# Performance work log

Measured on AMD Instinct MI355X. Metric: run time of the kernel, lower is better.

## Reference

```python
import jax, jax.numpy as jnp
import numpy as np

D_STATE = 16
D_CONV = 4


def rmsnorm(x, w, eps=1e-6):
    # normalize over last (channel) axis
    return x * jax.lax.rsqrt(jnp.mean(x * x, axis=-1, keepdims=True) + eps) * w


def silu(x):
    return x * jax.nn.sigmoid(x)


def mamba(x, in_proj_w, conv1d_w, conv1d_b, x_proj_w, dt_proj_w, dt_proj_b, A_log, D_param, out_proj_w):
    # x: [B, L, C], d_inner == C (expand=1)
    B, L, C = x.shape
    dt_rank = dt_proj_w.shape[1]
    xz = jnp.einsum('blc,ec->ble', x, in_proj_w)  # [B, L, 2C]
    u, z = jnp.split(xz, 2, axis=-1)
    # causal depthwise conv1d over time (pad left d_conv-1)
    uc = jax.lax.conv_general_dilated(
        u.transpose(0, 2, 1), conv1d_w[:, None, :], (1,), [(D_CONV - 1, 0)],
        dimension_numbers=('NCH', 'OIH', 'NCH'), feature_group_count=C)
    u = silu((uc + conv1d_b[None, :, None]).transpose(0, 2, 1))  # [B, L, C]
    x_dbl = jnp.einsum('blc,ec->ble', u, x_proj_w)  # [B, L, dt_rank + 2*N]
    dt, Bm, Cm = jnp.split(x_dbl, [dt_rank, dt_rank + D_STATE], axis=-1)
    delta = jax.nn.softplus(jnp.einsum('blr,dr->bld', dt, dt_proj_w) + dt_proj_b)  # [B, L, C]
    A = -jnp.exp(A_log)  # [C, N]
    deltaA = jnp.exp(delta[..., None] * A)              # [B, L, C, N]
    deltaBu = (delta * u)[..., None] * Bm[:, :, None, :]  # [B, L, C, N]

    def step(h, inp):
        dA, dBu, c = inp
        h = dA * h + dBu
        return h, jnp.einsum('bdn,bn->bd', h, c)

    h0 = jnp.zeros((B, C, D_STATE), x.dtype)
    _, ys = jax.lax.scan(step, h0, (deltaA.transpose(1, 0, 2, 3),
                                    deltaBu.transpose(1, 0, 2, 3),
                                    Cm.transpose(1, 0, 2)))
    y = ys.transpose(1, 0, 2) + u * D_param  # [B, L, C]
    y = y * silu(z)
    return jnp.einsum('bld,od->blo', y, out_proj_w)


def reference(x, norm_w, in_proj_w, conv1d_w, conv1d_b, x_proj_w, dt_proj_w, dt_proj_b,
              A_log, D_param, out_proj_w, scale_mod, dw_w, dw_b, res_scale):
    B, C, H, W = x.shape
    x_cl = x.transpose(0, 2, 3, 1)              # [B, H, W, C]
    xn_cl = rmsnorm(x_cl, norm_w)
    x_norm = xn_cl.transpose(0, 3, 1, 2)        # [B, C, H, W]
    # bidirectional Mamba over flattened spatial sequence
    x_flat = xn_cl.reshape(B, H * W, C)
    mparams = (in_proj_w, conv1d_w, conv1d_b, x_proj_w, dt_proj_w, dt_proj_b, A_log, D_param, out_proj_w)
    fwd = mamba(x_flat, *mparams)
    bwd = jnp.flip(mamba(jnp.flip(x_flat, axis=1), *mparams), axis=1)
    g = (fwd + bwd) * scale_mod
    global_feat = g.reshape(B, H, W, C).transpose(0, 3, 1, 2)
    # local spatial gating: sigmoid(depthwise 3x3 conv) * x_norm
    conv = jax.lax.conv_general_dilated(
        x_norm, dw_w[:, None, :, :], (1, 1), [(1, 1), (1, 1)],
        dimension_numbers=('NCHW', 'OIHW', 'NCHW'), feature_group_count=C)
    local_feat = jax.nn.sigmoid(conv + dw_b[None, :, None, None]) * x_norm
    return x + res_scale * (global_feat + local_feat)


def setup_inputs() -> dict:
    key = jax.random.key(0)
    ks = jax.random.split(key, 10)
    B, C, H, W = 8, 384, 32, 32
    dt_rank = 24  # ceil(384 / 16)
    s = 0.02
    f32 = jnp.float32
    return {
        'x': jax.random.normal(ks[0], (B, C, H, W), f32),
        'norm_w': jnp.ones((C,), f32),
        'in_proj_w': jax.random.normal(ks[1], (2 * C, C), f32) * s,
        'conv1d_w': jax.random.normal(ks[2], (C, D_CONV), f32) * 0.2,
        'conv1d_b': jnp.zeros((C,), f32),
        'x_proj_w': jax.random.normal(ks[3], (dt_rank + 2 * D_STATE, C), f32) * s,
        'dt_proj_w': jax.random.normal(ks[4], (C, dt_rank), f32) * 0.1,
        'dt_proj_b': jax.random.uniform(ks[5], (C,), f32, -4.0, -2.0),
        'A_log': jnp.log(jnp.tile(jnp.arange(1, D_STATE + 1, dtype=f32), (C, 1))),
        'D_param': jnp.ones((C,), f32),
        'out_proj_w': jax.random.normal(ks[6], (C, C), f32) * s,
        'scale_mod': jnp.full((1,), 0.25, f32),
        'dw_w': jax.random.normal(ks[7], (C, 3, 3), f32) * 0.1,
        'dw_b': jnp.zeros((C,), f32),
        'res_scale': jnp.full((1,), 0.5, f32),
    }
```

## Files before the change

kernel.cpp:

```cpp
#include <hip/hip_runtime.h>
#include <hip/hip_bf16.h>


typedef __attribute__((ext_vector_type(8))) short bf16x8;
typedef __attribute__((ext_vector_type(8))) unsigned short u16x8;
typedef __attribute__((ext_vector_type(4))) float f32x4;

#define L2E 1.44269504088896340736f

static __device__ __forceinline__ unsigned short f2bf(float f) {
  unsigned int u = __builtin_bit_cast(unsigned int, f);
  u += 0x7fff + ((u >> 16) & 1);
  return (unsigned short)(u >> 16);
}
static __device__ __forceinline__ float bf2f(unsigned short u) {
  unsigned int v = (unsigned int)u << 16;
  return __builtin_bit_cast(float, v);
}

#define GLOAD_LDS16(g, l)                                             \
  __builtin_amdgcn_global_load_lds(                                   \
      (const __attribute__((address_space(1))) unsigned int*)(g),     \
      (__attribute__((address_space(3))) unsigned int*)(l), 16, 0, 0)

__global__ __launch_bounds__(256) void prep_k(
    const float* __restrict__ in_w, const float* __restrict__ x_w,
    const float* __restrict__ dt_w, const float* __restrict__ out_w,
    const float* __restrict__ A_log, const float* __restrict__ nw,
    unsigned short* __restrict__ W_in, unsigned short* __restrict__ W_x,
    unsigned short* __restrict__ W_dt, unsigned short* __restrict__ W_out,
    float* __restrict__ A2) {
  int idx = blockIdx.x * 256 + threadIdx.x;
  switch (blockIdx.y) {
    case 0: if (idx < 768 * 384) W_in[idx] = f2bf(in_w[idx] * nw[idx % 384]); break;
    case 1: if (idx < 64 * 384) { int n = idx / 384, k = idx - n * 384;
              W_x[idx] = f2bf(n < 56 ? x_w[n * 384 + k] : 0.f); } break;
    case 2: if (idx < 384 * 32) { int n = idx >> 5, k = idx & 31;
              W_dt[idx] = f2bf(k < 24 ? dt_w[n * 24 + k] : 0.f); } break;
    case 3: if (idx < 384 * 384) W_out[idx] = f2bf(out_w[idx]); break;
    case 4: if (idx < 384 * 16) A2[idx] = -expf(A_log[idx]) * L2E; break;
  }
}

__global__ __launch_bounds__(256) void transpose_k(
    const float* __restrict__ x, unsigned short* __restrict__ xb,
    float* __restrict__ nf) {
  const int b = blockIdx.y;
  const int l0 = blockIdx.x * 32;
  const int tid = threadIdx.x;
  const int cr = tid >> 5, lw = tid & 31;
  const int cj = tid & 63, lr = tid >> 6;
  __shared__ float t64[64][33];
  __shared__ float part[8][33];
  float acc = 0.f;
  for (int cc = 0; cc < 6; ++cc) {
    #pragma unroll
    for (int k = 0; k < 8; ++k) {
      int cp = k * 8 + cr;
      int c = cc * 64 + cp;
      float v = x[(((size_t)(b * 384 + c)) << 10) + l0 + lw];
      t64[cp][lw] = v;
      acc = fmaf(v, v, acc);
    }
    __syncthreads();
    #pragma unroll
    for (int k2 = 0; k2 < 8; ++k2) {
      int ll = lr + 4 * k2;
      xb[((size_t)((b << 10) + l0 + ll)) * 384 + cc * 64 + cj] = f2bf(t64[cj][ll]);
    }
    __syncthreads();
  }
  part[cr][lw] = acc;
  __syncthreads();
  if (tid < 32) {
    float s = part[0][tid] + part[1][tid] + part[2][tid] + part[3][tid] +
              part[4][tid] + part[5][tid] + part[6][tid] + part[7][tid];
    nf[(b << 10) + l0 + tid] = rsqrtf(s * (1.f / 384.f) + 1e-6f);
  }
}

template <int EPI, int SUMIN>
__global__ __launch_bounds__(256) void gemm128_k(
    const unsigned short* __restrict__ A0u, const unsigned short* __restrict__ A1u,
    const unsigned short* __restrict__ Bw, int K, int N,
    float* __restrict__ outf, unsigned short* __restrict__ outb,
    const float* __restrict__ aux) {
  __shared__ __attribute__((aligned(16))) unsigned short As[128 * 32];
  __shared__ __attribute__((aligned(16))) unsigned short Bs[128 * 32];
  const int n0 = blockIdx.x * 128, m0 = blockIdx.y * 128;
  const int tid = threadIdx.x;
  const int lane = tid & 63, wave = tid >> 6;
  const int wm = wave >> 1, wn = wave & 1;
  const int fr = lane & 15, ks = (lane >> 4) * 8;
  const int row = tid >> 2, colseg = (tid & 3) * 8;
  const unsigned short* pA0 = A0u + (size_t)(m0 + row) * K + colseg;
  const unsigned short* pA1 = A0u + (size_t)(m0 + 64 + row) * K + colseg;
  const unsigned short* pB0 = Bw + (size_t)(n0 + row) * K + colseg;
  const unsigned short* pB1 = Bw + (size_t)(n0 + 64 + row) * K + colseg;
  unsigned short* lA0 = As + wave * 512;
  unsigned short* lA1 = As + 2048 + wave * 512;
  unsigned short* lB0 = Bs + wave * 512;
  unsigned short* lB1 = Bs + 2048 + wave * 512;
  f32x4 acc[4][4] = {};
  for (int k0 = 0; k0 < K; k0 += 32) {
    __syncthreads();
    if (SUMIN) {
      #pragma unroll
      for (int p = 0; p < 2; ++p) {
        int r = p * 64 + row;
        u16x8 va = *(const u16x8*)&A0u[(size_t)(m0 + r) * K + k0 + colseg];
        u16x8 vb = *(const u16x8*)&A1u[(size_t)(m0 + r) * K + k0 + colseg];
        u16x8 s;
        #pragma unroll
        for (int j = 0; j < 8; ++j) s[j] = f2bf(bf2f(va[j]) + bf2f(vb[j]));
        *(u16x8*)&As[r * 32 + colseg] = s;
      }
    } else {
      GLOAD_LDS16(pA0, lA0);
      GLOAD_LDS16(pA1, lA1);
      pA0 += 32; pA1 += 32;
    }
    GLOAD_LDS16(pB0, lB0);
    GLOAD_LDS16(pB1, lB1);
    pB0 += 32; pB1 += 32;
    __syncthreads();
    bf16x8 af[4], bf[4];
    #pragma unroll
    for (int mi = 0; mi < 4; ++mi)
      af[mi] = *(const bf16x8*)&As[(wm * 64 + mi * 16 + fr) * 32 + ks];
    #pragma unroll
    for (int ni = 0; ni < 4; ++ni)
      bf[ni] = *(const bf16x8*)&Bs[(wn * 64 + ni * 16 + fr) * 32 + ks];
    #pragma unroll
    for (int mi = 0; mi < 4; ++mi)
      #pragma unroll
      for (int ni = 0; ni < 4; ++ni)
        acc[mi][ni] = __builtin_amdgcn_mfma_f32_16x16x32_bf16(af[mi], bf[ni], acc[mi][ni], 0, 0, 0);
  }
  #pragma unroll
  for (int mi = 0; mi < 4; ++mi)
    #pragma unroll
    for (int ni = 0; ni < 4; ++ni)
      #pragma unroll
      for (int j = 0; j < 4; ++j) {
        int m = m0 + wm * 64 + mi * 16 + (lane >> 4) * 4 + j;
        int n = n0 + wn * 64 + ni * 16 + fr;
        float v = acc[mi][ni][j];
        if (EPI == 0) {
          outb[(size_t)m * N + n] = f2bf(v * aux[m]);
        } else {
          outf[(size_t)m * N + n] = v * aux[0];
        }
      }
}

template <int EPI>
__global__ __launch_bounds__(256) void gemm_k(
    const unsigned short* __restrict__ A0u, const unsigned short* __restrict__ A1u,
    const unsigned short* __restrict__ Bw, int K, int N,
    float* __restrict__ of0, float* __restrict__ of1,
    unsigned short* __restrict__ ob0, unsigned short* __restrict__ ob1,
    const float* __restrict__ aux) {
  const unsigned short* A = blockIdx.z ? A1u : A0u;
  float* outf = blockIdx.z ? of1 : of0;
  unsigned short* outb = blockIdx.z ? ob1 : ob0;
  __shared__ unsigned short As[64][40];
  __shared__ unsigned short Bs[64][40];
  const int n0 = blockIdx.x * 64, m0 = blockIdx.y * 64;
  const int tid = threadIdx.x;
  const int lane = tid & 63, wave = tid >> 6;
  const int wm = wave >> 1, wn = wave & 1;
  const int lrow = tid >> 2, lseg = (tid & 3) * 8;
  const int fr = lane & 15, ks = (lane >> 4) * 8;
  f32x4 acc[2][2] = {};
  for (int k0 = 0; k0 < K; k0 += 32) {
    __syncthreads();
    *(bf16x8*)&As[lrow][lseg] = *(const bf16x8*)&A[(size_t)(m0 + lrow) * K + k0 + lseg];
    *(bf16x8*)&Bs[lrow][lseg] = *(const bf16x8*)&Bw[(size_t)(n0 + lrow) * K + k0 + lseg];
    __syncthreads();
    bf16x8 a0 = *(const bf16x8*)&As[wm * 32 + fr][ks];
    bf16x8 a1 = *(const bf16x8*)&As[wm * 32 + 16 + fr][ks];
    bf16x8 b0 = *(const bf16x8*)&Bs[wn * 32 + fr][ks];
    bf16x8 b1 = *(const bf16x8*)&Bs[wn * 32 + 16 + fr][ks];
    acc[0][0] = __builtin_amdgcn_mfma_f32_16x16x32_bf16(a0, b0, acc[0][0], 0, 0, 0);
    acc[0][1] = __builtin_amdgcn_mfma_f32_16x16x32_bf16(a0, b1, acc[0][1], 0, 0, 0);
    acc[1][0] = __builtin_amdgcn_mfma_f32_16x16x32_bf16(a1, b0, acc[1][0], 0, 0, 0);
    acc[1][1] = __builtin_amdgcn_mfma_f32_16x16x32_bf16(a1, b1, acc[1][1], 0, 0, 0);
  }
  #pragma unroll
  for (int mi = 0; mi < 2; ++mi)
    #pragma unroll
    for (int ni = 0; ni < 2; ++ni)
      #pragma unroll
      for (int j = 0; j < 4; ++j) {
        int m = m0 + wm * 32 + mi * 16 + (lane >> 4) * 4 + j;
        int n = n0 + wn * 32 + ni * 16 + (lane & 15);
        float v = acc[mi][ni][j];
        if (EPI == 1) {
          if (n < 24) outb[m * 32 + n] = f2bf(v);
          else if (n < 32) outb[m * 32 + n] = 0;
          if (n >= 24 && n < 56) outf[m * 32 + (n - 24)] = v;
        } else {
          float t = v + aux[n];
          float sp = (t > 20.f) ? t : log1pf(expf(t));
          outb[(size_t)m * N + n] = f2bf(sp);
        }
      }
}

__global__ __launch_bounds__(384) void conv_silu_k(
    const unsigned short* __restrict__ xz, const float* __restrict__ cw,
    const float* __restrict__ cb,
    unsigned short* __restrict__ ub0, unsigned short* __restrict__ ub1) {
  const int st = blockIdx.x, b = blockIdx.y, dir = blockIdx.z;
  const int c = threadIdx.x;
  const int s0 = st * 8;
  const float w0 = cw[c * 4 + 0], w1 = cw[c * 4 + 1];
  const float w2 = cw[c * 4 + 2], w3 = cw[c * 4 + 3];
  const float bb = cb[c];
  unsigned short* ub = dir ? ub1 : ub0;
  float xv[11];
  #pragma unroll
  for (int k = 0; k < 11; ++k) {
    int j = s0 - 3 + k;
    float v = 0.f;
    if (j >= 0) {
      int t = dir ? (1023 - j) : j;
      v = bf2f(xz[(size_t)((b << 10) + t) * 768 + c]);
    }
    xv[k] = v;
  }
  #pragma unroll
  for (int s = 0; s < 8; ++s) {
    float a = bb + xv[s] * w0 + xv[s + 1] * w1 + xv[s + 2] * w2 + xv[s + 3] * w3;
    float uv = a * __builtin_amdgcn_rcpf(1.f + __builtin_amdgcn_exp2f(-a * L2E));
    ub[(size_t)((b << 10) + s0 + s) * 384 + c] = f2bf(uv);
  }
}

__global__ __launch_bounds__(512) void scan1_k(
    const unsigned short* __restrict__ de0, const unsigned short* __restrict__ de1,
    const unsigned short* __restrict__ ub0, const unsigned short* __restrict__ ub1,
    const float* __restrict__ bc0, const float* __restrict__ bc1,
    const float* __restrict__ A2, float* __restrict__ PH) {
  const int ct = blockIdx.x, b = blockIdx.y;
  const int dir = blockIdx.z >> 4, seg = blockIdx.z & 15;
  const unsigned short* del = dir ? de1 : de0;
  const unsigned short* uu  = dir ? ub1 : ub0;
  const float* bc  = dir ? bc1 : bc0;
  const int tid = threadIdx.x;
  const int lane = tid & 63, wave = tid >> 6;
  const int n = lane & 15, cg = lane >> 4;
  const int cl = wave * 4 + cg;
  const int c = ct * 32 + cl;
  const float a2 = A2[c * 16 + n];
  const size_t base = ((size_t)b << 10) + seg * 64;
  __shared__ __attribute__((aligned(16))) float sd[32][68];
  __shared__ __attribute__((aligned(16))) float su[32][68];
  __shared__ __attribute__((aligned(16))) float sB[16][68];
  const int li = tid >> 5, lj = tid & 31;
  const int li3 = tid >> 4, lj3 = tid & 15;
  unsigned short rd[4], ru[4];
  float rb[2];
  #pragma unroll
  for (int k = 0; k < 4; ++k) {
    size_t rowi = base + k * 16 + li;
    rd[k] = del[rowi * 384 + ct * 32 + lj];
    ru[k] = uu [rowi * 384 + ct * 32 + lj];
  }
  #pragma unroll
  for (int k = 0; k < 2; ++k)
    rb[k] = bc[(base + k * 32 + li3) * 32 + lj3];
  #pragma unroll
  for (int k = 0; k < 4; ++k) {
    sd[lj][k * 16 + li] = bf2f(rd[k]);
    su[lj][k * 16 + li] = bf2f(ru[k]);
  }
  #pragma unroll
  for (int k = 0; k < 2; ++k) sB[lj3][k * 32 + li3] = rb[k];
  __syncthreads();
  float h = 0.f, P = 1.f;
  for (int ch = 0; ch < 4; ++ch) {
    f32x4 dv[4], uv4[4], bmv[4];
    #pragma unroll
    for (int r = 0; r < 4; ++r) {
      dv[r]  = *(const f32x4*)&sd[cl][ch * 16 + r * 4];
      uv4[r] = *(const f32x4*)&su[cl][ch * 16 + r * 4];
      bmv[r] = *(const f32x4*)&sB[n][ch * 16 + r * 4];
    }
    #pragma unroll
    for (int i = 0; i < 16; ++i) {
      float dd = dv[i >> 2][i & 3];
      float dA = __builtin_amdgcn_exp2f(dd * a2);
      h = fmaf(dA, h, dd * uv4[i >> 2][i & 3] * bmv[i >> 2][i & 3]);
      P *= dA;
    }
  }
  size_t o = (size_t)((dir * 8 + b) * 16 + seg) * 6144 + c * 16 + n;
  *(float2*)&PH[o * 2] = make_float2(P, h);
}

__global__ __launch_bounds__(512) void scan2_k(
    const unsigned short* __restrict__ de0, const unsigned short* __restrict__ de1,
    const unsigned short* __restrict__ ub0, const unsigned short* __restrict__ ub1,
    const float* __restrict__ bc0, const float* __restrict__ bc1,
    const unsigned short* __restrict__ xz, const float* __restrict__ A2,
    const float* __restrict__ Dp, const float* __restrict__ PH,
    unsigned short* __restrict__ Sb0, unsigned short* __restrict__ Sb1) {
  const int ct = blockIdx.x, b = blockIdx.y;
  const int dir = blockIdx.z >> 4, seg = blockIdx.z & 15;
  const unsigned short* del = dir ? de1 : de0;
  const unsigned short* uu  = dir ? ub1 : ub0;
  const float* bc  = dir ? bc1 : bc0;
  unsigned short* S = dir ? Sb1 : Sb0;
  const int tid = threadIdx.x;
  const int lane = tid & 63, wave = tid >> 6;
  const int n = lane & 15, cg = lane >> 4;
  const int cl = wave * 4 + cg;
  const int c = ct * 32 + cl;
  const float a2 = A2[c * 16 + n];
  const float dpc = Dp[c];
  const size_t base = (size_t)b << 10;
  const int segoff = seg * 64;
  __shared__ __attribute__((aligned(16))) float sd[32][68];
  __shared__ __attribute__((aligned(16))) float su[32][68];
  __shared__ __attribute__((aligned(16))) float sz[32][68];
  __shared__ __attribute__((aligned(16))) float sbc[32][68];
  const int li = tid >> 5, lj = tid & 31;
  unsigned short rd[4], ru[4], rz[4];
  float rb[4];
  #pragma unroll
  for (int k = 0; k < 4; ++k) {
    size_t rowi = base + segoff + k * 16 + li;
    rd[k] = del[rowi * 384 + ct * 32 + lj];
    ru[k] = uu [rowi * 384 + ct * 32 + lj];
    int t = dir ? (1023 - (segoff + k * 16 + li)) : (segoff + k * 16 + li);
    rz[k] = xz[(base + t) * 768 + 384 + ct * 32 + lj];
    rb[k] = bc[rowi * 32 + lj];
  }
  float h = 0.f;
  {
    size_t rb2 = ((size_t)((dir * 8 + b) * 16) * 6144 + c * 16 + n) * 2;
    #pragma unroll
    for (int s = 0; s < 15; ++s) {
      float2 ph = *(const float2*)&PH[rb2 + (size_t)s * 12288];
      h = (s < seg) ? fmaf(ph.x, h, ph.y) : h;
    }
  }
  #pragma unroll
  for (int k = 0; k < 4; ++k) {
    sd[lj][k * 16 + li] = bf2f(rd[k]);
    su[lj][k * 16 + li] = bf2f(ru[k]);
    sz[lj][k * 16 + li] = bf2f(rz[k]);
    sbc[lj][k * 16 + li] = rb[k];
  }
  __syncthreads();
  for (int ch = 0; ch < 4; ++ch) {
    f32x4 dv[4], uv4[4], bmv[4], cmv[4];
    #pragma unroll
    for (int r = 0; r < 4; ++r) {
      dv[r]  = *(const f32x4*)&sd[cl][ch * 16 + r * 4];
      uv4[r] = *(const f32x4*)&su[cl][ch * 16 + r * 4];
      bmv[r] = *(const f32x4*)&sbc[n][ch * 16 + r * 4];
      cmv[r] = *(const f32x4*)&sbc[16 + n][ch * 16 + r * 4];
    }
    float p[16];
    #pragma unroll
    for (int i = 0; i < 16; ++i) {
      float dd = dv[i >> 2][i & 3];
      float dA = __builtin_amdgcn_exp2f(dd * a2);
      h = fmaf(dA, h, dd * uv4[i >> 2][i & 3] * bmv[i >> 2][i & 3]);
      p[i] = h * cmv[i >> 2][i & 3];
    }
    float q8[8];
    #pragma unroll
    for (int j = 0; j < 8; ++j) {
      float send = (n & 8) ? p[j] : p[j + 8];
      float recv = __shfl_xor(send, 8);
      float keep = (n & 8) ? p[j + 8] : p[j];
      q8[j] = keep + recv;
    }
    float q4[4];
    #pragma unroll
    for (int j = 0; j < 4; ++j) {
      float send = (n & 4) ? q8[j] : q8[j + 4];
      float recv = __shfl_xor(send, 4);
      float keep = (n & 4) ? q8[j + 4] : q8[j];
      q4[j] = keep + recv;
    }
    float q2[2];
    #pragma unroll
    for (int j = 0; j < 2; ++j) {
      float send = (n & 2) ? q4[j] : q4[j + 2];
      float recv = __shfl_xor(send, 2);
      float keep = (n & 2) ? q4[j + 2] : q4[j];
      q2[j] = keep + recv;
    }
    float send = (n & 1) ? q2[0] : q2[1];
    float recv = __shfl_xor(send, 1);
    float keep = (n & 1) ? q2[1] : q2[0];
    float ysum = keep + recv;
    float uvn = su[cl][ch * 16 + n];
    float zz  = sz[cl][ch * 16 + n];
    float sig = __builtin_amdgcn_rcpf(1.f + __builtin_amdgcn_exp2f(-zz * L2E));
    float y = (ysum + uvn * dpc) * (zz * sig);
    int s = segoff + ch * 16 + n;
    int t = dir ? (1023 - s) : s;
    S[(base + t) * 384 + c] = f2bf(y);
  }
}

__global__ __launch_bounds__(256) void final_k(
    const float* __restrict__ G, const unsigned short* __restrict__ xb,
    const float* __restrict__ nf, const float* __restrict__ nw,
    const float* __restrict__ x, const float* __restrict__ dww,
    const float* __restrict__ dwb, const float* __restrict__ rs,
    float* __restrict__ out) {
  __shared__ float tile[64][33];
  __shared__ float wq[9][64];
  __shared__ float bbs[64], nws[64];
  const int l0 = blockIdx.x * 32, c0 = blockIdx.y * 64, b = blockIdx.z;
  const int tid = threadIdx.x;
  for (int i = tid; i < 576; i += 256) {
    int c = i / 9, q = i - c * 9;
    wq[q][c] = dww[(size_t)(c0 + c) * 9 + q] * nw[c0 + c];
  }
  if (tid < 64) { bbs[tid] = dwb[c0 + tid]; nws[tid] = nw[c0 + tid]; }
  __syncthreads();
  {
    const int oct = tid & 7, li = tid >> 3;
    const int l = l0 + li;
    const int hh = l >> 5, ww = l & 31;
    float acc[8];
    {
      f32x4 ba = *(const f32x4*)&bbs[oct * 8];
      f32x4 bb2 = *(const f32x4*)&bbs[oct * 8 + 4];
      #pragma unroll
      for (int j = 0; j < 4; ++j) { acc[j] = ba[j]; acc[j + 4] = bb2[j]; }
    }
    #pragma unroll
    for (int di = -1; di <= 1; ++di) {
      int h2 = hh + di;
      if (h2 < 0 || h2 > 31) continue;
      #pragma unroll
      for (int dj = -1; dj <= 1; ++dj) {
        int w2 = ww + dj;
        if (w2 < 0 || w2 > 31) continue;
        int lp = h2 * 32 + w2;
        float nfl = nf[(b << 10) + lp];
        u16x8 v = *(const u16x8*)&xb[(size_t)((b << 10) + lp) * 384 + c0 + oct * 8];
        int q = (di + 1) * 3 + (dj + 1);
        f32x4 wa = *(const f32x4*)&wq[q][oct * 8];
        f32x4 wb = *(const f32x4*)&wq[q][oct * 8 + 4];
        #pragma unroll
        for (int j = 0; j < 4; ++j) {
          acc[j]     = fmaf(bf2f(v[j]) * nfl, wa[j], acc[j]);
          acc[j + 4] = fmaf(bf2f(v[j + 4]) * nfl, wb[j], acc[j + 4]);
        }
      }
    }
    size_t ri = (size_t)((b << 10) + l) * 384 + c0 + oct * 8;
    float nfl0 = nf[(b << 10) + l];
    u16x8 xc = *(const u16x8*)&xb[ri];
    f32x4 g0 = *(const f32x4*)&G[ri];
    f32x4 g1 = *(const f32x4*)&G[ri + 4];
    #pragma unroll
    for (int j = 0; j < 8; ++j) {
      float xv = bf2f(xc[j]) * nfl0 * nws[oct * 8 + j];
      float sig = __builtin_amdgcn_rcpf(1.f + __builtin_amdgcn_exp2f(-acc[j] * L2E));
      float gg = (j < 4) ? g0[j] : g1[j - 4];
      tile[oct * 8 + j][li] = gg + xv * sig;
    }
  }
  __syncthreads();
  {
    const int lw = tid & 31, cr = tid >> 5;
    const float rsv = rs[0];
    for (int p = 0; p < 8; ++p) {
      int c = c0 + p * 8 + cr;
      size_t o = ((size_t)(b * 384 + c) << 10) + l0 + lw;
      out[o] = x[o] + rsv * tile[p * 8 + cr][lw];
    }
  }
}

extern "C" void kernel_launch(void* const* d_in, const int* in_sizes, int n_in,
                              void* d_out, int out_size, void* d_ws, size_t ws_size,
                              hipStream_t stream) {
  const float* x         = (const float*)d_in[0];
  const float* norm_w    = (const float*)d_in[1];
  const float* in_proj_w = (const float*)d_in[2];
  const float* conv1d_w  = (const float*)d_in[3];
  const float* conv1d_b  = (const float*)d_in[4];
  const float* x_proj_w  = (const float*)d_in[5];
  const float* dt_proj_w = (const float*)d_in[6];
  const float* dt_proj_b = (const float*)d_in[7];
  const float* A_log     = (const float*)d_in[8];
  const float* D_param   = (const float*)d_in[9];
  const float* out_proj_w= (const float*)d_in[10];
  const float* scale_mod = (const float*)d_in[11];
  const float* dw_w      = (const float*)d_in[12];
  const float* dw_b      = (const float*)d_in[13];
  const float* res_scale = (const float*)d_in[14];
  float* out = (float*)d_out;

  char* base = (char*)d_ws;
  size_t off = 0;
  auto alloc = [&](size_t bytes) {
    off = (off + 255) & ~(size_t)255;
    void* p = base + off;
    off += bytes;
    return p;
  };
  const size_t B_BLC = (size_t)8192 * 384 * 2;

  unsigned short* xb   = (unsigned short*)alloc(B_BLC);
  float*          nf   = (float*)alloc((size_t)8192 * 4);
  unsigned short* xz   = (unsigned short*)alloc((size_t)8192 * 768 * 2);
  unsigned short* u_b0 = (unsigned short*)alloc(B_BLC);
  unsigned short* u_b1 = (unsigned short*)alloc(B_BLC);
  unsigned short* dtp0 = (unsigned short*)alloc((size_t)8192 * 32 * 2);
  unsigned short* dtp1 = (unsigned short*)alloc((size_t)8192 * 32 * 2);
  float*          bc0  = (float*)alloc((size_t)8192 * 32 * 4);
  float*          bc1  = (float*)alloc((size_t)8192 * 32 * 4);
  unsigned short* de0  = (unsigned short*)alloc(B_BLC);
  unsigned short* de1  = (unsigned short*)alloc(B_BLC);
  unsigned short* Sb0  = (unsigned short*)alloc(B_BLC);
  unsigned short* Sb1  = (unsigned short*)alloc(B_BLC);
  float*          PH   = (float*)alloc((size_t)1572864 * 2 * 4);
  unsigned short* W_in = (unsigned short*)alloc((size_t)768 * 384 * 2);
  unsigned short* W_x  = (unsigned short*)alloc((size_t)64 * 384 * 2);
  unsigned short* W_dt = (unsigned short*)alloc((size_t)384 * 32 * 2);
  unsigned short* W_out= (unsigned short*)alloc((size_t)384 * 384 * 2);
  float*          A2   = (float*)alloc((size_t)384 * 16 * 4);
  float*          G    = (float*)alloc((size_t)8192 * 384 * 4);

  prep_k<<<dim3(1152, 5), 256, 0, stream>>>(in_proj_w, x_proj_w, dt_proj_w,
                                            out_proj_w, A_log, norm_w,
                                            W_in, W_x, W_dt, W_out, A2);
  transpose_k<<<dim3(32, 8), 256, 0, stream>>>(x, xb, nf);
  gemm128_k<0, 0><<<dim3(6, 64), 256, 0, stream>>>(xb, xb, W_in, 384, 768,
                                                   nullptr, xz, nf);
  conv_silu_k<<<dim3(128, 8, 2), 384, 0, stream>>>(xz, conv1d_w, conv1d_b,
                                                   u_b0, u_b1);
  gemm_k<1><<<dim3(1, 128, 2), 256, 0, stream>>>(u_b0, u_b1, W_x, 384, 64,
                                                 bc0, bc1, dtp0, dtp1, nullptr);
  gemm_k<2><<<dim3(6, 128, 2), 256, 0, stream>>>(dtp0, dtp1, W_dt, 32, 384,
                                                 nullptr, nullptr, de0, de1,
                                                 dt_proj_b);
  scan1_k<<<dim3(12, 8, 32), 512, 0, stream>>>(de0, de1, u_b0, u_b1, bc0, bc1,
                                               A2, PH);
  scan2_k<<<dim3(12, 8, 32), 512, 0, stream>>>(de0, de1, u_b0, u_b1, bc0, bc1,
                                               xz, A2, D_param, PH, Sb0, Sb1);
  gemm128_k<3, 1><<<dim3(3, 64), 256, 0, stream>>>(Sb0, Sb1, W_out, 384, 384,
                                                   G, nullptr, scale_mod);
  final_k<<<dim3(32, 6, 8), 256, 0, stream>>>(G, xb, nf, norm_w, x, dw_w, dw_b,
                                              res_scale, out);
}
```

Measured before the change: 247.3 us.

## Fold dt projection into x_proj weights, bf16 scan staging, bf16 output GEMM

```diff
diff --git a/kernel.cpp b/kernel.cpp
--- a/kernel.cpp
+++ b/kernel.cpp
@@ -16,6 +16,12 @@
 static __device__ __forceinline__ float bf2f(unsigned short u) {
   unsigned int v = (unsigned int)u << 16;
   return __builtin_bit_cast(float, v);
+}
+static __device__ __forceinline__ float bfLO(unsigned int v) {
+  return __builtin_bit_cast(float, v << 16);
+}
+static __device__ __forceinline__ float bfHI(unsigned int v) {
+  return __builtin_bit_cast(float, v & 0xffff0000u);
 }
 
 #define GLOAD_LDS16(g, l)                                             \
@@ -28,17 +34,25 @@
     const float* __restrict__ dt_w, const float* __restrict__ out_w,
     const float* __restrict__ A_log, const float* __restrict__ nw,
     unsigned short* __restrict__ W_in, unsigned short* __restrict__ W_x,
-    unsigned short* __restrict__ W_dt, unsigned short* __restrict__ W_out,
+    unsigned short* __restrict__ W_out, unsigned short* __restrict__ Wde,
     float* __restrict__ A2) {
   int idx = blockIdx.x * 256 + threadIdx.x;
   switch (blockIdx.y) {
     case 0: if (idx < 768 * 384) W_in[idx] = f2bf(in_w[idx] * nw[idx % 384]); break;
     case 1: if (idx < 64 * 384) { int n = idx / 384, k = idx - n * 384;
-              W_x[idx] = f2bf(n < 56 ? x_w[n * 384 + k] : 0.f); } break;
-    case 2: if (idx < 384 * 32) { int n = idx >> 5, k = idx & 31;
-              W_dt[idx] = f2bf(k < 24 ? dt_w[n * 24 + k] : 0.f); } break;
-    case 3: if (idx < 384 * 384) W_out[idx] = f2bf(out_w[idx]); break;
-    case 4: if (idx < 384 * 16) A2[idx] = -expf(A_log[idx]) * L2E; break;
+              W_x[idx] = f2bf(n < 32 ? x_w[(24 + n) * 384 + k] : 0.f); } break;
+    case 2: if (idx < 384 * 384) W_out[idx] = f2bf(out_w[idx]); break;
+    case 3: if (idx < 384 * 16) A2[idx] = -expf(A_log[idx]) * L2E; break;
+    case 4: case 5: {
+      int i2 = (blockIdx.y - 4) * 294912 + idx;
+      if (i2 < 384 * 384) {
+        int o = i2 / 384, c = i2 - o * 384;
+        float s = 0.f;
+        #pragma unroll
+        for (int r = 0; r < 24; ++r) s += dt_w[o * 24 + r] * x_w[r * 384 + c];
+        Wde[i2] = f2bf(s);
+      }
+    } break;
   }
 }
 
@@ -83,8 +97,10 @@
 __global__ __launch_bounds__(256) void gemm128_k(
     const unsigned short* __restrict__ A0u, const unsigned short* __restrict__ A1u,
     const unsigned short* __restrict__ Bw, int K, int N,
-    float* __restrict__ outf, unsigned short* __restrict__ outb,
+    unsigned short* __restrict__ ob0, unsigned short* __restrict__ ob1,
     const float* __restrict__ aux) {
+  const unsigned short* Au = (EPI == 2 && blockIdx.z) ? A1u : A0u;
+  unsigned short* ob = (EPI == 2 && blockIdx.z) ? ob1 : ob0;
   __shared__ __attribute__((aligned(16))) unsigned short As[128 * 32];
   __shared__ __attribute__((aligned(16))) unsigned short Bs[128 * 32];
   const int n0 = blockIdx.x * 128, m0 = blockIdx.y * 128;
@@ -93,8 +109,8 @@
   const int wm = wave >> 1, wn = wave & 1;
   const int fr = lane & 15, ks = (lane >> 4) * 8;
   const int row = tid >> 2, colseg = (tid & 3) * 8;
-  const unsigned short* pA0 = A0u + (size_t)(m0 + row) * K + colseg;
-  const unsigned short* pA1 = A0u + (size_t)(m0 + 64 + row) * K + colseg;
+  const unsigned short* pA0 = Au + (size_t)(m0 + row) * K + colseg;
+  const unsigned short* pA1 = Au + (size_t)(m0 + 64 + row) * K + colseg;
   const unsigned short* pB0 = Bw + (size_t)(n0 + row) * K + colseg;
   const unsigned short* pB1 = Bw + (size_t)(n0 + 64 + row) * K + colseg;
   unsigned short* lA0 = As + wave * 512;
@@ -124,18 +140,18 @@
     GLOAD_LDS16(pB1, lB1);
     pB0 += 32; pB1 += 32;
     __syncthreads();
-    bf16x8 af[4], bf[4];
+    bf16x8 af[4], bfr[4];
     #pragma unroll
     for (int mi = 0; mi < 4; ++mi)
       af[mi] = *(const bf16x8*)&As[(wm * 64 + mi * 16 + fr) * 32 + ks];
     #pragma unroll
     for (int ni = 0; ni < 4; ++ni)
-      bf[ni] = *(const bf16x8*)&Bs[(wn * 64 + ni * 16 + fr) * 32 + ks];
+      bfr[ni] = *(const bf16x8*)&Bs[(wn * 64 + ni * 16 + fr) * 32 + ks];
     #pragma unroll
     for (int mi = 0; mi < 4; ++mi)
       #pragma unroll
       for (int ni = 0; ni < 4; ++ni)
-        acc[mi][ni] = __builtin_amdgcn_mfma_f32_16x16x32_bf16(af[mi], bf[ni], acc[mi][ni], 0, 0, 0);
+        acc[mi][ni] = __builtin_amdgcn_mfma_f32_16x16x32_bf16(af[mi], bfr[ni], acc[mi][ni], 0, 0, 0);
   }
   #pragma unroll
   for (int mi = 0; mi < 4; ++mi)
@@ -147,26 +163,26 @@
         int n = n0 + wn * 64 + ni * 16 + fr;
         float v = acc[mi][ni][j];
         if (EPI == 0) {
-          outb[(size_t)m * N + n] = f2bf(v * aux[m]);
+          ob0[(size_t)m * N + n] = f2bf(v * aux[m]);
+        } else if (EPI == 2) {
+          float t = v + aux[n];
+          float sp = (t > 20.f) ? t : log1pf(expf(t));
+          ob[(size_t)m * N + n] = f2bf(sp);
         } else {
-          outf[(size_t)m * N + n] = v * aux[0];
+          ob0[(size_t)m * N + n] = f2bf(v * aux[0]);
         }
       }
 }
 
-template <int EPI>
-__global__ __launch_bounds__(256) void gemm_k(
+__global__ __launch_bounds__(256) void gemm_bc_k(
     const unsigned short* __restrict__ A0u, const unsigned short* __restrict__ A1u,
-    const unsigned short* __restrict__ Bw, int K, int N,
-    float* __restrict__ of0, float* __restrict__ of1,
-    unsigned short* __restrict__ ob0, unsigned short* __restrict__ ob1,
-    const float* __restrict__ aux) {
+    const unsigned short* __restrict__ Bw, int K,
+    float* __restrict__ of0, float* __restrict__ of1) {
   const unsigned short* A = blockIdx.z ? A1u : A0u;
   float* outf = blockIdx.z ? of1 : of0;
-  unsigned short* outb = blockIdx.z ? ob1 : ob0;
   __shared__ unsigned short As[64][40];
   __shared__ unsigned short Bs[64][40];
-  const int n0 = blockIdx.x * 64, m0 = blockIdx.y * 64;
+  const int m0 = blockIdx.y * 64;
   const int tid = threadIdx.x;
   const int lane = tid & 63, wave = tid >> 6;
   const int wm = wave >> 1, wn = wave & 1;
@@ -176,7 +192,7 @@
   for (int k0 = 0; k0 < K; k0 += 32) {
     __syncthreads();
     *(bf16x8*)&As[lrow][lseg] = *(const bf16x8*)&A[(size_t)(m0 + lrow) * K + k0 + lseg];
-    *(bf16x8*)&Bs[lrow][lseg] = *(const bf16x8*)&Bw[(size_t)(n0 + lrow) * K + k0 + lseg];
+    *(bf16x8*)&Bs[lrow][lseg] = *(const bf16x8*)&Bw[(size_t)lrow * K + k0 + lseg];
     __syncthreads();
     bf16x8 a0 = *(const bf16x8*)&As[wm * 32 + fr][ks];
     bf16x8 a1 = *(const bf16x8*)&As[wm * 32 + 16 + fr][ks];
@@ -194,17 +210,8 @@
       #pragma unroll
       for (int j = 0; j < 4; ++j) {
         int m = m0 + wm * 32 + mi * 16 + (lane >> 4) * 4 + j;
-        int n = n0 + wn * 32 + ni * 16 + (lane & 15);
-        float v = acc[mi][ni][j];
-        if (EPI == 1) {
-          if (n < 24) outb[m * 32 + n] = f2bf(v);
-          else if (n < 32) outb[m * 32 + n] = 0;
-          if (n >= 24 && n < 56) outf[m * 32 + (n - 24)] = v;
-        } else {
-          float t = v + aux[n];
-          float sp = (t > 20.f) ? t : log1pf(expf(t));
-          outb[(size_t)m * N + n] = f2bf(sp);
-        }
+        int n = wn * 32 + ni * 16 + (lane & 15);
+        if (n < 32) outf[m * 32 + n] = acc[mi][ni][j];
       }
 }
 
@@ -238,7 +245,7 @@
   }
 }
 
-__global__ __launch_bounds__(512) void scan1_k(
+__global__ __launch_bounds__(512, 4) void scan1_k(
     const unsigned short* __restrict__ de0, const unsigned short* __restrict__ de1,
     const unsigned short* __restrict__ ub0, const unsigned short* __restrict__ ub1,
     const float* __restrict__ bc0, const float* __restrict__ bc1,
@@ -255,52 +262,57 @@
   const int c = ct * 32 + cl;
   const float a2 = A2[c * 16 + n];
   const size_t base = ((size_t)b << 10) + seg * 64;
-  __shared__ __attribute__((aligned(16))) float sd[32][68];
-  __shared__ __attribute__((aligned(16))) float su[32][68];
-  __shared__ __attribute__((aligned(16))) float sB[16][68];
-  const int li = tid >> 5, lj = tid & 31;
-  const int li3 = tid >> 4, lj3 = tid & 15;
-  unsigned short rd[4], ru[4];
-  float rb[2];
-  #pragma unroll
-  for (int k = 0; k < 4; ++k) {
-    size_t rowi = base + k * 16 + li;
-    rd[k] = del[rowi * 384 + ct * 32 + lj];
-    ru[k] = uu [rowi * 384 + ct * 32 + lj];
-  }
-  #pragma unroll
-  for (int k = 0; k < 2; ++k)
-    rb[k] = bc[(base + k * 32 + li3) * 32 + lj3];
-  #pragma unroll
-  for (int k = 0; k < 4; ++k) {
-    sd[lj][k * 16 + li] = bf2f(rd[k]);
-    su[lj][k * 16 + li] = bf2f(ru[k]);
-  }
-  #pragma unroll
-  for (int k = 0; k < 2; ++k) sB[lj3][k * 32 + li3] = rb[k];
+  __shared__ __attribute__((aligned(16))) unsigned int sd[32 * 36];
+  __shared__ __attribute__((aligned(16))) unsigned int sdu[32 * 36];
+  __shared__ __attribute__((aligned(16))) unsigned int sB[16 * 36];
+  {
+    const int li = tid >> 5, lj = tid & 31;
+    unsigned short* sd16 = (unsigned short*)sd;
+    unsigned short* sdu16 = (unsigned short*)sdu;
+    #pragma unroll
+    for (int k = 0; k < 4; ++k) {
+      size_t rowi = base + k * 16 + li;
+      unsigned short rd = del[rowi * 384 + ct * 32 + lj];
+      unsigned short ru = uu [rowi * 384 + ct * 32 + lj];
+      sd16[lj * 72 + k * 16 + li] = rd;
+      sdu16[lj * 72 + k * 16 + li] = f2bf(bf2f(rd) * bf2f(ru));
+    }
+    const int li2 = tid >> 4, lj2 = tid & 15;
+    unsigned short* sB16 = (unsigned short*)sB;
+    #pragma unroll
+    for (int k = 0; k < 2; ++k) {
+      size_t rowi = base + k * 32 + li2;
+      sB16[lj2 * 72 + k * 32 + li2] = f2bf(bc[rowi * 32 + lj2]);
+    }
+  }
   __syncthreads();
-  float h = 0.f, P = 1.f;
-  for (int ch = 0; ch < 4; ++ch) {
-    f32x4 dv[4], uv4[4], bmv[4];
-    #pragma unroll
-    for (int r = 0; r < 4; ++r) {
-      dv[r]  = *(const f32x4*)&sd[cl][ch * 16 + r * 4];
-      uv4[r] = *(const f32x4*)&su[cl][ch * 16 + r * 4];
-      bmv[r] = *(const f32x4*)&sB[n][ch * 16 + r * 4];
-    }
-    #pragma unroll
-    for (int i = 0; i < 16; ++i) {
-      float dd = dv[i >> 2][i & 3];
-      float dA = __builtin_amdgcn_exp2f(dd * a2);
-      h = fmaf(dA, h, dd * uv4[i >> 2][i & 3] * bmv[i >> 2][i & 3]);
-      P *= dA;
-    }
-  }
+  float hA = 0.f, hB = 0.f, suf = 0.f;
+  for (int ch = 3; ch >= 0; --ch) {
+    uint4 qa = *(const uint4*)&sd[cl * 36 + ch * 8];
+    uint4 qb = *(const uint4*)&sd[cl * 36 + ch * 8 + 4];
+    uint4 ra = *(const uint4*)&sdu[cl * 36 + ch * 8];
+    uint4 rb = *(const uint4*)&sdu[cl * 36 + ch * 8 + 4];
+    uint4 ba = *(const uint4*)&sB[n * 36 + ch * 8];
+    uint4 bb = *(const uint4*)&sB[n * 36 + ch * 8 + 4];
+    unsigned int pd[8] = {qa.x, qa.y, qa.z, qa.w, qb.x, qb.y, qb.z, qb.w};
+    unsigned int pu[8] = {ra.x, ra.y, ra.z, ra.w, rb.x, rb.y, rb.z, rb.w};
+    unsigned int pb[8] = {ba.x, ba.y, ba.z, ba.w, bb.x, bb.y, bb.z, bb.w};
+    #pragma unroll
+    for (int j = 7; j >= 0; --j) {
+      float e1 = __builtin_amdgcn_exp2f(a2 * suf);
+      hA = fmaf(e1, bfHI(pu[j]) * bfHI(pb[j]), hA);
+      suf += bfHI(pd[j]);
+      float e0 = __builtin_amdgcn_exp2f(a2 * suf);
+      hB = fmaf(e0, bfLO(pu[j]) * bfLO(pb[j]), hB);
+      suf += bfLO(pd[j]);
+    }
+  }
+  float P = __builtin_amdgcn_exp2f(a2 * suf);
   size_t o = (size_t)((dir * 8 + b) * 16 + seg) * 6144 + c * 16 + n;
-  *(float2*)&PH[o * 2] = make_float2(P, h);
-}
-
-__global__ __launch_bounds__(512) void scan2_k(
+  *(float2*)&PH[o * 2] = make_float2(P, hA + hB);
+}
+
+__global__ __launch_bounds__(512, 4) void scan2_k(
     const unsigned short* __restrict__ de0, const unsigned short* __restrict__ de1,
     const unsigned short* __restrict__ ub0, const unsigned short* __restrict__ ub1,
     const float* __restrict__ bc0, const float* __restrict__ bc1,
@@ -320,57 +332,71 @@
   const int c = ct * 32 + cl;
   const float a2 = A2[c * 16 + n];
   const float dpc = Dp[c];
-  const size_t base = (size_t)b << 10;
+  const size_t bb_ = (size_t)b << 10;
   const int segoff = seg * 64;
-  __shared__ __attribute__((aligned(16))) float sd[32][68];
-  __shared__ __attribute__((aligned(16))) float su[32][68];
-  __shared__ __attribute__((aligned(16))) float sz[32][68];
-  __shared__ __attribute__((aligned(16))) float sbc[32][68];
-  const int li = tid >> 5, lj = tid & 31;
-  unsigned short rd[4], ru[4], rz[4];
-  float rb[4];
-  #pragma unroll
-  for (int k = 0; k < 4; ++k) {
-    size_t rowi = base + segoff + k * 16 + li;
-    rd[k] = del[rowi * 384 + ct * 32 + lj];
-    ru[k] = uu [rowi * 384 + ct * 32 + lj];
-    int t = dir ? (1023 - (segoff + k * 16 + li)) : (segoff + k * 16 + li);
-    rz[k] = xz[(base + t) * 768 + 384 + ct * 32 + lj];
-    rb[k] = bc[rowi * 32 + lj];
-  }
+  __shared__ __attribute__((aligned(16))) unsigned int sd[32 * 36];
+  __shared__ __attribute__((aligned(16))) unsigned int su[32 * 36];
+  __shared__ __attribute__((aligned(16))) unsigned int sz[32 * 36];
+  __shared__ __attribute__((aligned(16))) unsigned int sb[16 * 36];
+  __shared__ __attribute__((aligned(16))) unsigned int sc[16 * 36];
+  __shared__ __attribute__((aligned(16))) unsigned short sy[64 * 36];
   float h = 0.f;
   {
-    size_t rb2 = ((size_t)((dir * 8 + b) * 16) * 6144 + c * 16 + n) * 2;
+    size_t rb2 = (((size_t)(dir * 8 + b) * 16) * 6144 + c * 16 + n) * 2;
     #pragma unroll
     for (int s = 0; s < 15; ++s) {
       float2 ph = *(const float2*)&PH[rb2 + (size_t)s * 12288];
       h = (s < seg) ? fmaf(ph.x, h, ph.y) : h;
     }
   }
-  #pragma unroll
-  for (int k = 0; k < 4; ++k) {
-    sd[lj][k * 16 + li] = bf2f(rd[k]);
-    su[lj][k * 16 + li] = bf2f(ru[k]);
-    sz[lj][k * 16 + li] = bf2f(rz[k]);
-    sbc[lj][k * 16 + li] = rb[k];
+  {
+    const int li = tid >> 5, lj = tid & 31;
+    unsigned short* sd16 = (unsigned short*)sd;
+    unsigned short* su16 = (unsigned short*)su;
+    unsigned short* sz16 = (unsigned short*)sz;
+    #pragma unroll
+    for (int k = 0; k < 4; ++k) {
+      size_t rowi = bb_ + segoff + k * 16 + li;
+      sd16[lj * 72 + k * 16 + li] = del[rowi * 384 + ct * 32 + lj];
+      su16[lj * 72 + k * 16 + li] = uu [rowi * 384 + ct * 32 + lj];
+      int tz = dir ? (1023 - (segoff + k * 16 + li)) : (segoff + k * 16 + li);
+      sz16[lj * 72 + k * 16 + li] = xz[(bb_ + tz) * 768 + 384 + ct * 32 + lj];
+    }
+    const int li2 = tid >> 4, lj2 = tid & 15;
+    unsigned short* sb16 = (unsigned short*)sb;
+    unsigned short* sc16 = (unsigned short*)sc;
+    #pragma unroll
+    for (int k = 0; k < 2; ++k) {
+      size_t rowi = bb_ + segoff + k * 32 + li2;
+      sb16[lj2 * 72 + k * 32 + li2] = f2bf(bc[rowi * 32 + lj2]);
+      sc16[lj2 * 72 + k * 32 + li2] = f2bf(bc[rowi * 32 + 16 + lj2]);
+    }
   }
   __syncthreads();
   for (int ch = 0; ch < 4; ++ch) {
-    f32x4 dv[4], uv4[4], bmv[4], cmv[4];
-    #pragma unroll
-    for (int r = 0; r < 4; ++r) {
-      dv[r]  = *(const f32x4*)&sd[cl][ch * 16 + r * 4];
-      uv4[r] = *(const f32x4*)&su[cl][ch * 16 + r * 4];
-      bmv[r] = *(const f32x4*)&sbc[n][ch * 16 + r * 4];
-      cmv[r] = *(const f32x4*)&sbc[16 + n][ch * 16 + r * 4];
-    }
+    uint4 qa = *(const uint4*)&sd[cl * 36 + ch * 8];
+    uint4 qb = *(const uint4*)&sd[cl * 36 + ch * 8 + 4];
+    uint4 ra = *(const uint4*)&su[cl * 36 + ch * 8];
+    uint4 rb = *(const uint4*)&su[cl * 36 + ch * 8 + 4];
+    uint4 ba = *(const uint4*)&sb[n * 36 + ch * 8];
+    uint4 bb2 = *(const uint4*)&sb[n * 36 + ch * 8 + 4];
+    uint4 ca = *(const uint4*)&sc[n * 36 + ch * 8];
+    uint4 cb = *(const uint4*)&sc[n * 36 + ch * 8 + 4];
+    unsigned int pd[8] = {qa.x, qa.y, qa.z, qa.w, qb.x, qb.y, qb.z, qb.w};
+    unsigned int pu[8] = {ra.x, ra.y, ra.z, ra.w, rb.x, rb.y, rb.z, rb.w};
+    unsigned int pb[8] = {ba.x, ba.y, ba.z, ba.w, bb2.x, bb2.y, bb2.z, bb2.w};
+    unsigned int pc[8] = {ca.x, ca.y, ca.z, ca.w, cb.x, cb.y, cb.z, cb.w};
     float p[16];
     #pragma unroll
-    for (int i = 0; i < 16; ++i) {
-      float dd = dv[i >> 2][i & 3];
-      float dA = __builtin_amdgcn_exp2f(dd * a2);
-      h = fmaf(dA, h, dd * uv4[i >> 2][i & 3] * bmv[i >> 2][i & 3]);
-      p[i] = h * cmv[i >> 2][i & 3];
+    for (int j = 0; j < 8; ++j) {
+      float dL = bfLO(pd[j]);
+      float dA = __builtin_amdgcn_exp2f(dL * a2);
+      h = fmaf(dA, h, dL * bfLO(pu[j]) * bfLO(pb[j]));
+      p[2 * j] = h * bfLO(pc[j]);
+      float dH = bfHI(pd[j]);
+      dA = __builtin_amdgcn_exp2f(dH * a2);
+      h = fmaf(dA, h, dH * bfHI(pu[j]) * bfHI(pb[j]));
+      p[2 * j + 1] = h * bfHI(pc[j]);
     }
     float q8[8];
     #pragma unroll
@@ -400,18 +426,24 @@
     float recv = __shfl_xor(send, 1);
     float keep = (n & 1) ? q2[1] : q2[0];
     float ysum = keep + recv;
-    float uvn = su[cl][ch * 16 + n];
-    float zz  = sz[cl][ch * 16 + n];
+    float uvn = bf2f(((const unsigned short*)su)[cl * 72 + ch * 16 + n]);
+    float zz  = bf2f(((const unsigned short*)sz)[cl * 72 + ch * 16 + n]);
     float sig = __builtin_amdgcn_rcpf(1.f + __builtin_amdgcn_exp2f(-zz * L2E));
     float y = (ysum + uvn * dpc) * (zz * sig);
-    int s = segoff + ch * 16 + n;
-    int t = dir ? (1023 - s) : s;
-    S[(base + t) * 384 + c] = f2bf(y);
+    sy[(ch * 16 + n) * 36 + cl] = f2bf(y);
+  }
+  __syncthreads();
+  {
+    const int t = tid >> 3, cq = (tid & 7) * 4;
+    int tg = segoff + t;
+    int trow = dir ? (1023 - tg) : tg;
+    *(ushort4*)&S[(bb_ + trow) * 384 + ct * 32 + cq] =
+        *(const ushort4*)&sy[t * 36 + cq];
   }
 }
 
 __global__ __launch_bounds__(256) void final_k(
-    const float* __restrict__ G, const unsigned short* __restrict__ xb,
+    const unsigned short* __restrict__ Gb, const unsigned short* __restrict__ xb,
     const float* __restrict__ nf, const float* __restrict__ nw,
     const float* __restrict__ x, const float* __restrict__ dww,
     const float* __restrict__ dwb, const float* __restrict__ rs,
@@ -462,14 +494,12 @@
     size_t ri = (size_t)((b << 10) + l) * 384 + c0 + oct * 8;
     float nfl0 = nf[(b << 10) + l];
     u16x8 xc = *(const u16x8*)&xb[ri];
-    f32x4 g0 = *(const f32x4*)&G[ri];
-    f32x4 g1 = *(const f32x4*)&G[ri + 4];
+    u16x8 gv = *(const u16x8*)&Gb[ri];
     #pragma unroll
     for (int j = 0; j < 8; ++j) {
       float xv = bf2f(xc[j]) * nfl0 * nws[oct * 8 + j];
       float sig = __builtin_amdgcn_rcpf(1.f + __builtin_amdgcn_exp2f(-acc[j] * L2E));
-      float gg = (j < 4) ? g0[j] : g1[j - 4];
-      tile[oct * 8 + j][li] = gg + xv * sig;
+      tile[oct * 8 + j][li] = bf2f(gv[j]) + xv * sig;
     }
   }
   __syncthreads();
@@ -519,8 +549,6 @@
   unsigned short* xz   = (unsigned short*)alloc((size_t)8192 * 768 * 2);
   unsigned short* u_b0 = (unsigned short*)alloc(B_BLC);
   unsigned short* u_b1 = (unsigned short*)alloc(B_BLC);
-  unsigned short* dtp0 = (unsigned short*)alloc((size_t)8192 * 32 * 2);
-  unsigned short* dtp1 = (unsigned short*)alloc((size_t)8192 * 32 * 2);
   float*          bc0  = (float*)alloc((size_t)8192 * 32 * 4);
   float*          bc1  = (float*)alloc((size_t)8192 * 32 * 4);
   unsigned short* de0  = (unsigned short*)alloc(B_BLC);
@@ -530,30 +558,29 @@
   float*          PH   = (float*)alloc((size_t)1572864 * 2 * 4);
   unsigned short* W_in = (unsigned short*)alloc((size_t)768 * 384 * 2);
   unsigned short* W_x  = (unsigned short*)alloc((size_t)64 * 384 * 2);
-  unsigned short* W_dt = (unsigned short*)alloc((size_t)384 * 32 * 2);
   unsigned short* W_out= (unsigned short*)alloc((size_t)384 * 384 * 2);
+  unsigned short* Wde  = (unsigned short*)alloc((size_t)384 * 384 * 2);
   float*          A2   = (float*)alloc((size_t)384 * 16 * 4);
-  float*          G    = (float*)alloc((size_t)8192 * 384 * 4);
-
-  prep_k<<<dim3(1152, 5), 256, 0, stream>>>(in_proj_w, x_proj_w, dt_proj_w,
+  unsigned short* Gb   = (unsigned short*)alloc(B_BLC);
+
+  prep_k<<<dim3(1152, 6), 256, 0, stream>>>(in_proj_w, x_proj_w, dt_proj_w,
                                             out_proj_w, A_log, norm_w,
-                                            W_in, W_x, W_dt, W_out, A2);
+                                            W_in, W_x, W_out, Wde, A2);
   transpose_k<<<dim3(32, 8), 256, 0, stream>>>(x, xb, nf);
   gemm128_k<0, 0><<<dim3(6, 64), 256, 0, stream>>>(xb, xb, W_in, 384, 768,
-                                                   nullptr, xz, nf);
+                                                   xz, xz, nf);
   conv_silu_k<<<dim3(128, 8, 2), 384, 0, stream>>>(xz, conv1d_w, conv1d_b,
                                                    u_b0, u_b1);
-  gemm_k<1><<<dim3(1, 128, 2), 256, 0, stream>>>(u_b0, u_b1, W_x, 384, 64,
-                                                 bc0, bc1, dtp0, dtp1, nullptr);
-  gemm_k<2><<<dim3(6, 128, 2), 256, 0, stream>>>(dtp0, dtp1, W_dt, 32, 384,
-                                                 nullptr, nullptr, de0, de1,
-                                                 dt_proj_b);
+  gemm_bc_k<<<dim3(1, 128, 2), 256, 0, stream>>>(u_b0, u_b1, W_x, 384,
+                                                 bc0, bc1);
+  gemm128_k<2, 0><<<dim3(3, 64, 2), 256, 0, stream>>>(u_b0, u_b1, Wde, 384, 384,
+                                                      de0, de1, dt_proj_b);
   scan1_k<<<dim3(12, 8, 32), 512, 0, stream>>>(de0, de1, u_b0, u_b1, bc0, bc1,
                                                A2, PH);
   scan2_k<<<dim3(12, 8, 32), 512, 0, stream>>>(de0, de1, u_b0, u_b1, bc0, bc1,
                                                xz, A2, D_param, PH, Sb0, Sb1);
   gemm128_k<3, 1><<<dim3(3, 64), 256, 0, stream>>>(Sb0, Sb1, W_out, 384, 384,
-                                                   G, nullptr, scale_mod);
-  final_k<<<dim3(32, 6, 8), 256, 0, stream>>>(G, xb, nf, norm_w, x, dw_w, dw_b,
+                                                   Gb, Gb, scale_mod);
+  final_k<<<dim3(32, 6, 8), 256, 0, stream>>>(Gb, xb, nf, norm_w, x, dw_w, dw_b,
                                               res_scale, out);
 }
```

Result: slower. 276.4 us (+11.7%).
